# Kernel optimization log

Hardware: AMD Instinct MI355X
Metric: run time of the kernel (lower is better)

The kernel has to match this reference:

```python
import jax, jax.numpy as jnp
import numpy as np
from jax import lax

N, H, W, C = 64, 256, 256, 16  # NHWC input
O, K = 16, 3                   # out_channels, kern_size


def setup_inputs() -> dict:
    key = jax.random.key(0)
    k_in, k_u, k_v, k_w = jax.random.split(key, 4)
    # glorot_normal std for shape [fan_in, fan_out]-ish 2D weights: sqrt(2/(a+b))
    u = jax.random.normal(k_u, (O, K), dtype=jnp.float32) * np.sqrt(2.0 / (O + K)).astype(np.float32)
    v = jax.random.normal(k_v, (O, K), dtype=jnp.float32) * np.sqrt(2.0 / (O + K)).astype(np.float32)
    w = jax.random.normal(k_w, (O, C), dtype=jnp.float32) * np.sqrt(2.0 / (O + C)).astype(np.float32)
    b = jnp.zeros((O,), dtype=jnp.float32)
    inputs = jax.random.normal(k_in, (N, H, W, C), dtype=jnp.float32)
    return {"inputs": inputs, "u": u, "v": v, "w": w, "b": b}


def reference(inputs, u, v, w, b):
    # CP low-rank kernel construction: kern[i,j,k,l] = v[l,i] * u[l,j] * w[l,k]
    # -> HWIO kernel of shape [K, K, C, O]
    kern = jnp.einsum('lj,lk,li->ijkl', u, w, v)
    out = lax.conv_general_dilated(
        inputs, kern,
        window_strides=(1, 1),
        padding='SAME',
        dimension_numbers=('NHWC', 'HWIO', 'NHWC'),
    )
    return jax.nn.relu(out + b)
```

## Files before the change

kernel.cpp:

```cpp
#include <hip/hip_runtime.h>
#include <hip/hip_bf16.h>

#define N_ 64
#define H_ 256
#define W_ 256
#define C_ 16
#define O_ 16

#define TW 32
#define TH 8
#define HALO_W (TW + 2)
#define HALO_H (TH + 2)
#define NHALO (HALO_W * HALO_H)


__global__ __launch_bounds__(256, 7)
void sep_conv_kernel(const float* __restrict__ in,
                     const float* __restrict__ u,
                     const float* __restrict__ v,
                     const float* __restrict__ w,
                     const float* __restrict__ b,
                     float* __restrict__ out) {
    __shared__ float4 t_lds[4 * NHALO];

    const int tid = threadIdx.x;
    const int x0 = blockIdx.x * TW;
    const int y0 = blockIdx.y * TH;
    const int n  = blockIdx.z;

    const float* inbase = in + (size_t)n * H_ * W_ * C_;

    const int p0 = tid;
    const int p1 = tid + 256;
    const bool has1 = (p1 < NHALO);

    const int r0 = p0 / HALO_W, c0 = p0 - r0 * HALO_W;
    const int r1 = p1 / HALO_W, c1 = p1 - r1 * HALO_W;
    const int gy0 = y0 + r0 - 1, gx0 = x0 + c0 - 1;
    const int gy1 = y0 + r1 - 1, gx1 = x0 + c1 - 1;
    const bool in0 = (unsigned)gy0 < (unsigned)H_ && (unsigned)gx0 < (unsigned)W_;
    const bool in1 = has1 && (unsigned)gy1 < (unsigned)H_ && (unsigned)gx1 < (unsigned)W_;

    float4 A[4], B[4];
    #pragma unroll
    for (int q = 0; q < 4; ++q) A[q] = make_float4(0.f, 0.f, 0.f, 0.f);
    #pragma unroll
    for (int q = 0; q < 4; ++q) B[q] = make_float4(0.f, 0.f, 0.f, 0.f);

    if (in0) {
        const float4* s4 = (const float4*)(inbase + ((size_t)gy0 * W_ + gx0) * C_);
        #pragma unroll
        for (int q = 0; q < 4; ++q) A[q] = s4[q];
    }
    if (in1) {
        const float4* s4 = (const float4*)(inbase + ((size_t)gy1 * W_ + gx1) * C_);
        #pragma unroll
        for (int q = 0; q < 4; ++q) B[q] = s4[q];
    }

    {
        const float iv0[16] = {A[0].x, A[0].y, A[0].z, A[0].w,
                               A[1].x, A[1].y, A[1].z, A[1].w,
                               A[2].x, A[2].y, A[2].z, A[2].w,
                               A[3].x, A[3].y, A[3].z, A[3].w};
        float tv[16];
        #pragma unroll
        for (int l = 0; l < 16; ++l) {
            float s = 0.f;
            #pragma unroll
            for (int k = 0; k < 16; ++k) s = fmaf(w[l * 16 + k], iv0[k], s);
            tv[l] = s;
        }
        t_lds[0 * NHALO + p0] = make_float4(tv[0],  tv[1],  tv[2],  tv[3]);
        t_lds[1 * NHALO + p0] = make_float4(tv[4],  tv[5],  tv[6],  tv[7]);
        t_lds[2 * NHALO + p0] = make_float4(tv[8],  tv[9],  tv[10], tv[11]);
        t_lds[3 * NHALO + p0] = make_float4(tv[12], tv[13], tv[14], tv[15]);
    }
    if (has1) {
        const float iv1[16] = {B[0].x, B[0].y, B[0].z, B[0].w,
                               B[1].x, B[1].y, B[1].z, B[1].w,
                               B[2].x, B[2].y, B[2].z, B[2].w,
                               B[3].x, B[3].y, B[3].z, B[3].w};
        float tv[16];
        #pragma unroll
        for (int l = 0; l < 16; ++l) {
            float s = 0.f;
            #pragma unroll
            for (int k = 0; k < 16; ++k) s = fmaf(w[l * 16 + k], iv1[k], s);
            tv[l] = s;
        }
        t_lds[0 * NHALO + p1] = make_float4(tv[0],  tv[1],  tv[2],  tv[3]);
        t_lds[1 * NHALO + p1] = make_float4(tv[4],  tv[5],  tv[6],  tv[7]);
        t_lds[2 * NHALO + p1] = make_float4(tv[8],  tv[9],  tv[10], tv[11]);
        t_lds[3 * NHALO + p1] = make_float4(tv[12], tv[13], tv[14], tv[15]);
    }
    __syncthreads();

    const int tx = tid & (TW - 1);
    const int ty = tid >> 5;

    float acc[16];
    #pragma unroll
    for (int l = 0; l < 16; ++l) acc[l] = 0.f;

    #pragma unroll
    for (int i = 0; i < 3; ++i) {
        float h[16];
        #pragma unroll
        for (int l = 0; l < 16; ++l) h[l] = 0.f;
        #pragma unroll
        for (int j = 0; j < 3; ++j) {
            const int p = (ty + i) * HALO_W + (tx + j);
            const float4 a0 = t_lds[0 * NHALO + p];
            const float4 a1 = t_lds[1 * NHALO + p];
            const float4 a2 = t_lds[2 * NHALO + p];
            const float4 a3 = t_lds[3 * NHALO + p];
            const float tvv[16] = {a0.x, a0.y, a0.z, a0.w,
                                   a1.x, a1.y, a1.z, a1.w,
                                   a2.x, a2.y, a2.z, a2.w,
                                   a3.x, a3.y, a3.z, a3.w};
            #pragma unroll
            for (int l = 0; l < 16; ++l) {
                h[l] = fmaf(u[l * 3 + j], tvv[l], h[l]);
            }
        }
        #pragma unroll
        for (int l = 0; l < 16; ++l) {
            acc[l] = fmaf(v[l * 3 + i], h[l], acc[l]);
        }
    }

    float r[16];
    #pragma unroll
    for (int l = 0; l < 16; ++l) {
        float val = acc[l] + b[l];
        r[l] = val > 0.f ? val : 0.f;
    }
    float4* o4 = (float4*)(out + (((size_t)n * H_ + (y0 + ty)) * W_ + (x0 + tx)) * C_);
    o4[0] = make_float4(r[0],  r[1],  r[2],  r[3]);
    o4[1] = make_float4(r[4],  r[5],  r[6],  r[7]);
    o4[2] = make_float4(r[8],  r[9],  r[10], r[11]);
    o4[3] = make_float4(r[12], r[13], r[14], r[15]);
}

extern "C" void kernel_launch(void* const* d_in, const int* in_sizes, int n_in,
                              void* d_out, int out_size, void* d_ws, size_t ws_size,
                              hipStream_t stream) {
    const float* in = (const float*)d_in[0];
    const float* u  = (const float*)d_in[1];
    const float* v  = (const float*)d_in[2];
    const float* w  = (const float*)d_in[3];
    const float* b  = (const float*)d_in[4];
    float* out = (float*)d_out;

    dim3 grid(W_ / TW, H_ / TH, N_);
    dim3 block(256);
    sep_conv_kernel<<<grid, block, 0, stream>>>(in, u, v, w, b, out);
}
```

Before: 457.9 us.

## Stream rows per block with rolling separable-filter registers and double-buffered LDS

Each block now owns a full image-row width and walks a 16-row strip. Per row it computes the channel mix once, writes it to a double-buffered LDS row, and applies the horizontal 3-tap filter. The vertical 3-tap filter is applied from rolling registers holding the previous, current and next rows. This removes the halo recomputation of the 2D tiles (only 2 extra rows per 16-row strip instead of a 10x34 halo for 8x32 outputs) and prefetches the next input row from global memory during compute. The cost is one barrier per row, more registers (launch bounds lowered to 4), and fewer blocks (1024), which reduces parallelism.

```diff
diff --git a/kernel.cpp b/kernel.cpp
--- a/kernel.cpp
+++ b/kernel.cpp
@@ -1,5 +1,4 @@
 #include <hip/hip_runtime.h>
-#include <hip/hip_bf16.h>
 
 #define N_ 64
 #define H_ 256
@@ -7,140 +6,142 @@
 #define C_ 16
 #define O_ 16
 
-#define TW 32
-#define TH 8
-#define HALO_W (TW + 2)
-#define HALO_H (TH + 2)
-#define NHALO (HALO_W * HALO_H)
+#define CH 16
+#define PLANE 258
 
 
-__global__ __launch_bounds__(256, 7)
+__device__ __forceinline__ void load_row(const float* __restrict__ base, int r, int x,
+                                         float4 pf[4]) {
+    const float4* s4 = (const float4*)(base + ((size_t)r * W_ + x) * C_);
+    #pragma unroll
+    for (int q = 0; q < 4; ++q) pf[q] = s4[q];
+}
+
+__device__ __forceinline__ void cmix(const float* __restrict__ w, const float4 pf[4],
+                                     float tn[16]) {
+    const float iv[16] = {pf[0].x, pf[0].y, pf[0].z, pf[0].w,
+                          pf[1].x, pf[1].y, pf[1].z, pf[1].w,
+                          pf[2].x, pf[2].y, pf[2].z, pf[2].w,
+                          pf[3].x, pf[3].y, pf[3].z, pf[3].w};
+    #pragma unroll
+    for (int l = 0; l < 16; ++l) {
+        float s = 0.f;
+        #pragma unroll
+        for (int k = 0; k < 16; ++k) s = fmaf(w[l * 16 + k], iv[k], s);
+        tn[l] = s;
+    }
+}
+
+__device__ __forceinline__ void write_t(float4* __restrict__ lds, int slot, int x,
+                                        const float tn[16]) {
+    #pragma unroll
+    for (int q = 0; q < 4; ++q)
+        lds[(slot * 4 + q) * PLANE + (x + 1)] =
+            make_float4(tn[4 * q], tn[4 * q + 1], tn[4 * q + 2], tn[4 * q + 3]);
+}
+
+__device__ __forceinline__ void hrow(const float4* __restrict__ lds, int slot, int x,
+                                     const float* __restrict__ u, const float tn[16],
+                                     float h[16]) {
+    float4 m4[4], p4[4];
+    #pragma unroll
+    for (int q = 0; q < 4; ++q) {
+        m4[q] = lds[(slot * 4 + q) * PLANE + x];
+        p4[q] = lds[(slot * 4 + q) * PLANE + x + 2];
+    }
+    const float tm[16] = {m4[0].x, m4[0].y, m4[0].z, m4[0].w,
+                          m4[1].x, m4[1].y, m4[1].z, m4[1].w,
+                          m4[2].x, m4[2].y, m4[2].z, m4[2].w,
+                          m4[3].x, m4[3].y, m4[3].z, m4[3].w};
+    const float tp[16] = {p4[0].x, p4[0].y, p4[0].z, p4[0].w,
+                          p4[1].x, p4[1].y, p4[1].z, p4[1].w,
+                          p4[2].x, p4[2].y, p4[2].z, p4[2].w,
+                          p4[3].x, p4[3].y, p4[3].z, p4[3].w};
+    #pragma unroll
+    for (int l = 0; l < 16; ++l)
+        h[l] = fmaf(u[l * 3 + 0], tm[l],
+               fmaf(u[l * 3 + 2], tp[l], u[l * 3 + 1] * tn[l]));
+}
+
+__global__ __launch_bounds__(256, 4)
 void sep_conv_kernel(const float* __restrict__ in,
                      const float* __restrict__ u,
                      const float* __restrict__ v,
                      const float* __restrict__ w,
                      const float* __restrict__ b,
                      float* __restrict__ out) {
-    __shared__ float4 t_lds[4 * NHALO];
+    __shared__ float4 t_lds[2 * 4 * PLANE];
 
-    const int tid = threadIdx.x;
-    const int x0 = blockIdx.x * TW;
-    const int y0 = blockIdx.y * TH;
-    const int n  = blockIdx.z;
+    const int x  = threadIdx.x;
+    const int y0 = blockIdx.x * CH;
+    const int n  = blockIdx.y;
 
-    const float* inbase = in + (size_t)n * H_ * W_ * C_;
+    const float* inb  = in  + (size_t)n * H_ * W_ * C_;
+    float*       outb = out + (size_t)n * H_ * W_ * C_;
 
-    const int p0 = tid;
-    const int p1 = tid + 256;
-    const bool has1 = (p1 < NHALO);
-
-    const int r0 = p0 / HALO_W, c0 = p0 - r0 * HALO_W;
-    const int r1 = p1 / HALO_W, c1 = p1 - r1 * HALO_W;
-    const int gy0 = y0 + r0 - 1, gx0 = x0 + c0 - 1;
-    const int gy1 = y0 + r1 - 1, gx1 = x0 + c1 - 1;
-    const bool in0 = (unsigned)gy0 < (unsigned)H_ && (unsigned)gx0 < (unsigned)W_;
-    const bool in1 = has1 && (unsigned)gy1 < (unsigned)H_ && (unsigned)gx1 < (unsigned)W_;
-
-    float4 A[4], B[4];
-    #pragma unroll
-    for (int q = 0; q < 4; ++q) A[q] = make_float4(0.f, 0.f, 0.f, 0.f);
-    #pragma unroll
-    for (int q = 0; q < 4; ++q) B[q] = make_float4(0.f, 0.f, 0.f, 0.f);
-
-    if (in0) {
-        const float4* s4 = (const float4*)(inbase + ((size_t)gy0 * W_ + gx0) * C_);
-        #pragma unroll
-        for (int q = 0; q < 4; ++q) A[q] = s4[q];
-    }
-    if (in1) {
-        const float4* s4 = (const float4*)(inbase + ((size_t)gy1 * W_ + gx1) * C_);
-        #pragma unroll
-        for (int q = 0; q < 4; ++q) B[q] = s4[q];
+    if (x < 16) {
+        const int slot = x >> 3, q = (x >> 1) & 3, side = x & 1;
+        t_lds[(slot * 4 + q) * PLANE + (side ? PLANE - 1 : 0)] =
+            make_float4(0.f, 0.f, 0.f, 0.f);
     }
 
-    {
-        const float iv0[16] = {A[0].x, A[0].y, A[0].z, A[0].w,
-                               A[1].x, A[1].y, A[1].z, A[1].w,
-                               A[2].x, A[2].y, A[2].z, A[2].w,
-                               A[3].x, A[3].y, A[3].z, A[3].w};
-        float tv[16];
+    float4 pf[4];
+    float tn[16], hp[16], hc[16], hn[16];
+
+    const int rm1 = y0 - 1;
+    const bool have_m1 = (rm1 >= 0);
+    if (have_m1) {
+        load_row(inb, rm1, x, pf);
+        cmix(w, pf, tn);
+    }
+    load_row(inb, y0, x, pf);
+    if (have_m1) write_t(t_lds, rm1 & 1, x, tn);
+    __syncthreads();
+    if (have_m1) {
+        hrow(t_lds, rm1 & 1, x, u, tn, hp);
+    } else {
+        #pragma unroll
+        for (int l = 0; l < 16; ++l) hp[l] = 0.f;
+    }
+
+    cmix(w, pf, tn);
+    load_row(inb, y0 + 1, x, pf);
+    write_t(t_lds, y0 & 1, x, tn);
+    __syncthreads();
+    hrow(t_lds, y0 & 1, x, u, tn, hc);
+
+    for (int yy = 0; yy < CH; ++yy) {
+        const int y  = y0 + yy;
+        const int rn = y + 1;
+        if (rn < H_) {
+            cmix(w, pf, tn);
+            if (yy + 1 < CH && rn + 1 < H_)
+                load_row(inb, rn + 1, x, pf);
+            write_t(t_lds, rn & 1, x, tn);
+            __syncthreads();
+            hrow(t_lds, rn & 1, x, u, tn, hn);
+        } else {
+            #pragma unroll
+            for (int l = 0; l < 16; ++l) hn[l] = 0.f;
+        }
+
+        float r[16];
         #pragma unroll
         for (int l = 0; l < 16; ++l) {
-            float s = 0.f;
-            #pragma unroll
-            for (int k = 0; k < 16; ++k) s = fmaf(w[l * 16 + k], iv0[k], s);
-            tv[l] = s;
+            float val = fmaf(v[l * 3 + 0], hp[l],
+                        fmaf(v[l * 3 + 1], hc[l],
+                        fmaf(v[l * 3 + 2], hn[l], b[l])));
+            r[l] = fmaxf(val, 0.f);
         }
-        t_lds[0 * NHALO + p0] = make_float4(tv[0],  tv[1],  tv[2],  tv[3]);
-        t_lds[1 * NHALO + p0] = make_float4(tv[4],  tv[5],  tv[6],  tv[7]);
-        t_lds[2 * NHALO + p0] = make_float4(tv[8],  tv[9],  tv[10], tv[11]);
-        t_lds[3 * NHALO + p0] = make_float4(tv[12], tv[13], tv[14], tv[15]);
+        float4* o4 = (float4*)(outb + ((size_t)y * W_ + x) * C_);
+        o4[0] = make_float4(r[0],  r[1],  r[2],  r[3]);
+        o4[1] = make_float4(r[4],  r[5],  r[6],  r[7]);
+        o4[2] = make_float4(r[8],  r[9],  r[10], r[11]);
+        o4[3] = make_float4(r[12], r[13], r[14], r[15]);
+
+        #pragma unroll
+        for (int l = 0; l < 16; ++l) { hp[l] = hc[l]; hc[l] = hn[l]; }
     }
-    if (has1) {
-        const float iv1[16] = {B[0].x, B[0].y, B[0].z, B[0].w,
-                               B[1].x, B[1].y, B[1].z, B[1].w,
-                               B[2].x, B[2].y, B[2].z, B[2].w,
-                               B[3].x, B[3].y, B[3].z, B[3].w};
-        float tv[16];
-        #pragma unroll
-        for (int l = 0; l < 16; ++l) {
-            float s = 0.f;
-            #pragma unroll
-            for (int k = 0; k < 16; ++k) s = fmaf(w[l * 16 + k], iv1[k], s);
-            tv[l] = s;
-        }
-        t_lds[0 * NHALO + p1] = make_float4(tv[0],  tv[1],  tv[2],  tv[3]);
-        t_lds[1 * NHALO + p1] = make_float4(tv[4],  tv[5],  tv[6],  tv[7]);
-        t_lds[2 * NHALO + p1] = make_float4(tv[8],  tv[9],  tv[10], tv[11]);
-        t_lds[3 * NHALO + p1] = make_float4(tv[12], tv[13], tv[14], tv[15]);
-    }
-    __syncthreads();
-
-    const int tx = tid & (TW - 1);
-    const int ty = tid >> 5;
-
-    float acc[16];
-    #pragma unroll
-    for (int l = 0; l < 16; ++l) acc[l] = 0.f;
-
-    #pragma unroll
-    for (int i = 0; i < 3; ++i) {
-        float h[16];
-        #pragma unroll
-        for (int l = 0; l < 16; ++l) h[l] = 0.f;
-        #pragma unroll
-        for (int j = 0; j < 3; ++j) {
-            const int p = (ty + i) * HALO_W + (tx + j);
-            const float4 a0 = t_lds[0 * NHALO + p];
-            const float4 a1 = t_lds[1 * NHALO + p];
-            const float4 a2 = t_lds[2 * NHALO + p];
-            const float4 a3 = t_lds[3 * NHALO + p];
-            const float tvv[16] = {a0.x, a0.y, a0.z, a0.w,
-                                   a1.x, a1.y, a1.z, a1.w,
-                                   a2.x, a2.y, a2.z, a2.w,
-                                   a3.x, a3.y, a3.z, a3.w};
-            #pragma unroll
-            for (int l = 0; l < 16; ++l) {
-                h[l] = fmaf(u[l * 3 + j], tvv[l], h[l]);
-            }
-        }
-        #pragma unroll
-        for (int l = 0; l < 16; ++l) {
-            acc[l] = fmaf(v[l * 3 + i], h[l], acc[l]);
-        }
-    }
-
-    float r[16];
-    #pragma unroll
-    for (int l = 0; l < 16; ++l) {
-        float val = acc[l] + b[l];
-        r[l] = val > 0.f ? val : 0.f;
-    }
-    float4* o4 = (float4*)(out + (((size_t)n * H_ + (y0 + ty)) * W_ + (x0 + tx)) * C_);
-    o4[0] = make_float4(r[0],  r[1],  r[2],  r[3]);
-    o4[1] = make_float4(r[4],  r[5],  r[6],  r[7]);
-    o4[2] = make_float4(r[8],  r[9],  r[10], r[11]);
-    o4[3] = make_float4(r[12], r[13], r[14], r[15]);
 }
 
 extern "C" void kernel_launch(void* const* d_in, const int* in_sizes, int n_in,
@@ -153,7 +154,7 @@
     const float* b  = (const float*)d_in[4];
     float* out = (float*)d_out;
 
-    dim3 grid(W_ / TW, H_ / TH, N_);
+    dim3 grid(H_ / CH, N_);
     dim3 block(256);
     sep_conv_kernel<<<grid, block, 0, stream>>>(in, u, v, w, b, out);
 }
```

Result: no change. 464.5 us (+1.4%).
